# Kernel optimization log

Measured on AMD Instinct MI355X. Metric: run time of the kernel, lower is better.

The kernel has to match this reference:

```python
import jax, jax.numpy as jnp
import numpy as np

W_SIM, W_REC, W_FREQ, W_IMP, W_TYPE = 0.45, 0.2, 0.15, 0.1, 0.1
TYPE_WEIGHT = 0.9
DECAY_HALF_LIFE = 200.0
TEMPERATURE = 0.07
LN_EPS = 1e-5


def _l2norm(v, axis=-1):
    # matches torch F.normalize (eps=1e-12 clamp on the norm)
    n = jnp.linalg.norm(v, axis=axis, keepdims=True)
    return v / jnp.maximum(n, 1e-12)


def setup_inputs() -> dict:
    key = jax.random.key(0)
    ks = jax.random.split(key, 8)
    B, D, S = 16384, 2048, 64
    s = 1.0 / np.sqrt(D)
    x = jax.random.normal(ks[0], (B, D), jnp.float32)
    prototypes = _l2norm(jax.random.normal(ks[1], (S, D), jnp.float32))
    proto_conf = jax.random.uniform(ks[2], (S,), jnp.float32)
    proto_age = jax.random.uniform(ks[3], (S,), jnp.float32)
    proto_evidence = jnp.ones((S,), jnp.float32)
    W_in = jax.random.normal(ks[4], (D, D), jnp.float32) * s
    b_in = jnp.zeros((D,), jnp.float32)
    Wr1 = jax.random.normal(ks[5], (D // 2, D), jnp.float32) * s
    br1 = jnp.zeros((D // 2,), jnp.float32)
    Wr2 = jax.random.normal(ks[6], (4, D // 2), jnp.float32) * (1.0 / np.sqrt(D // 2))
    br2 = jnp.zeros((4,), jnp.float32)
    W_out = jax.random.normal(ks[7], (D, 2 * D), jnp.float32) * (1.0 / np.sqrt(2 * D))
    b_out = jnp.zeros((D,), jnp.float32)
    ln_w = jnp.ones((D,), jnp.float32)
    ln_b = jnp.zeros((D,), jnp.float32)
    return {"x": x, "prototypes": prototypes, "proto_conf": proto_conf,
            "proto_age": proto_age, "proto_evidence": proto_evidence,
            "W_in": W_in, "b_in": b_in, "Wr1": Wr1, "br1": br1,
            "Wr2": Wr2, "br2": br2, "W_out": W_out, "b_out": b_out,
            "ln_w": ln_w, "ln_b": ln_b}


def reference(x, prototypes, proto_conf, proto_age, proto_evidence,
              W_in, b_in, Wr1, br1, Wr2, br2, W_out, b_out, ln_w, ln_b):
    S = prototypes.shape[0]
    protos_per_type = S // 4

    # in_proj + normalize
    h = x @ W_in.T + b_in                                  # [B, D]
    h_norm = _l2norm(h)

    # type router: Linear -> GELU(exact) -> Linear -> softmax
    r = jax.nn.gelu(x @ Wr1.T + br1, approximate=False)    # [B, D/2]
    type_weights = jax.nn.softmax(r @ Wr2.T + br2, axis=-1)  # [B, 4]

    # prototype similarity
    p_norm = _l2norm(prototypes)
    raw_sim = h_norm @ p_norm.T                            # [B, S]

    type_assign = jnp.arange(S) // protos_per_type         # [S] in {0..3}
    type_mask = type_weights[:, type_assign]               # [B, S]
    weighted_sim = raw_sim * type_mask * proto_conf[None, :]

    # multi-factor salience (fused elementwise)
    recency = jnp.exp(-proto_age / DECAY_HALF_LIFE)[None, :]
    freq_norm = (jnp.log(proto_evidence + 1.0) /
                 (jnp.log(proto_evidence.max() + 2.0) + 1e-8))[None, :]
    sal = (W_SIM * weighted_sim + W_REC * recency + W_FREQ * freq_norm
           + W_IMP * proto_conf[None, :] + W_TYPE * TYPE_WEIGHT)
    sal = jnp.clip(sal, 0.0, 1.0)

    # attention over prototype bank
    attn = jax.nn.softmax(sal / TEMPERATURE, axis=-1)       # [B, S]
    retrieved = attn @ prototypes                           # [B, D]

    combined = jnp.concatenate([x, retrieved], axis=-1)     # [B, 2D]
    out = jax.nn.gelu(combined @ W_out.T + b_out, approximate=False)
    # dropout is identity in eval mode

    # residual + LayerNorm (biased variance, eps=1e-5)
    y = out + x
    mu = jnp.mean(y, axis=-1, keepdims=True)
    var = jnp.mean((y - mu) ** 2, axis=-1, keepdims=True)
    return ln_w * (y - mu) / jnp.sqrt(var + LN_EPS) + ln_b
```

## Files before the change

kernel.cpp:

```cpp
#include <hip/hip_runtime.h>
#include <hip/hip_bf16.h>
#include <cstdint>

#define DEV __device__ __forceinline__

typedef __bf16 bf16x8 __attribute__((ext_vector_type(8)));
typedef float f32x4 __attribute__((ext_vector_type(4)));
typedef unsigned short ushort_t;
typedef ushort_t ushort8 __attribute__((ext_vector_type(8)));

DEV ushort_t f2bf(float f) {
  union { float f; uint32_t u; } x; x.f = f;
  uint32_t r = (x.u + 0x7fffu + ((x.u >> 16) & 1u)) >> 16;
  return (ushort_t)r;
}
DEV float bf2f(ushort_t b) {
  union { uint32_t u; float f; } x; x.u = ((uint32_t)b) << 16;
  return x.f;
}
DEV float gelu_exact(float v) {
  return 0.5f * v * (1.0f + erff(v * 0.70710678118654752f));
}
DEV void gload_lds16(const void* g, void* l) {
  __builtin_amdgcn_global_load_lds(
      (const __attribute__((address_space(1))) void*)g,
      (__attribute__((address_space(3))) void*)l, 16, 0, 0);
}


__global__ __launch_bounds__(64) void prep_scal(
    const float* __restrict__ conf, const float* __restrict__ age,
    const float* __restrict__ ev, float* __restrict__ base, float* __restrict__ cs) {
  int l = threadIdx.x;
  float e = ev[l];
  float m = e;
  #pragma unroll
  for (int d = 1; d < 64; d <<= 1) m = fmaxf(m, __shfl_xor(m, d));
  float freq = logf(e + 1.f) / (logf(m + 2.f) + 1e-8f);
  base[l] = 0.2f * expf(-age[l] * (1.f / 200.f)) + 0.15f * freq + 0.1f * conf[l] + 0.09f;
  cs[l] = 0.45f * conf[l];
}

__global__ __launch_bounds__(256) void prep_pnorm(
    const float* __restrict__ protos, const float* __restrict__ b_in,
    float* __restrict__ p_norm, float* __restrict__ dvec) {
  const int s = blockIdx.x, t = threadIdx.x;
  const float* p = protos + (size_t)s * 2048;
  float vals[8];
  float ss = 0.f, sb = 0.f;
  #pragma unroll
  for (int ii = 0; ii < 2; ++ii) {
    float4 v = *(const float4*)(p + t * 8 + ii * 4);
    float4 bi = *(const float4*)(b_in + t * 8 + ii * 4);
    vals[ii * 4 + 0] = v.x; vals[ii * 4 + 1] = v.y; vals[ii * 4 + 2] = v.z; vals[ii * 4 + 3] = v.w;
    ss += v.x * v.x + v.y * v.y + v.z * v.z + v.w * v.w;
    sb += v.x * bi.x + v.y * bi.y + v.z * bi.z + v.w * bi.w;
  }
  #pragma unroll
  for (int d = 1; d < 64; d <<= 1) { ss += __shfl_xor(ss, d); sb += __shfl_xor(sb, d); }
  __shared__ float red[8];
  if ((t & 63) == 0) { red[t >> 6] = ss; red[4 + (t >> 6)] = sb; }
  __syncthreads();
  ss = red[0] + red[1] + red[2] + red[3];
  sb = red[4] + red[5] + red[6] + red[7];
  float inv = 1.f / fmaxf(sqrtf(ss), 1e-12f);
  #pragma unroll
  for (int k = 0; k < 8; ++k) p_norm[(size_t)s * 2048 + t * 8 + k] = vals[k] * inv;
  if (t == 0) dvec[s] = sb * inv;
}


__global__ __launch_bounds__(256) void conv_x(const float* __restrict__ x, ushort_t* __restrict__ xa) {
  size_t e = ((size_t)blockIdx.x * 256 + threadIdx.x) * 8;
  int row = (int)(e >> 11), col = (int)(e & 2047);
  float4 f0 = *(const float4*)(x + e);
  float4 f1 = *(const float4*)(x + e + 4);
  ushort8 o;
  o[0] = f2bf(f0.x); o[1] = f2bf(f0.y); o[2] = f2bf(f0.z); o[3] = f2bf(f0.w);
  o[4] = f2bf(f1.x); o[5] = f2bf(f1.y); o[6] = f2bf(f1.z); o[7] = f2bf(f1.w);
  *(ushort8*)(xa + (size_t)row * 2112 + col) = o;
}

__global__ __launch_bounds__(256) void conv_wbig(const float* __restrict__ W_in,
                                                 const float* __restrict__ Wr1,
                                                 ushort_t* __restrict__ wbig) {
  size_t e = ((size_t)blockIdx.x * 256 + threadIdx.x) * 8;
  int row = (int)(e >> 11), col = (int)(e & 2047);
  if (row >= 3072 && row < 3136) return;
  ushort8 o;
  if (row < 3072) {
    const float* src = (row < 2048) ? (W_in + (size_t)row * 2048 + col)
                                    : (Wr1 + (size_t)(row - 2048) * 2048 + col);
    float4 f0 = *(const float4*)(src);
    float4 f1 = *(const float4*)(src + 4);
    o[0] = f2bf(f0.x); o[1] = f2bf(f0.y); o[2] = f2bf(f0.z); o[3] = f2bf(f0.w);
    o[4] = f2bf(f1.x); o[5] = f2bf(f1.y); o[6] = f2bf(f1.z); o[7] = f2bf(f1.w);
  } else {
    o = ushort8{0, 0, 0, 0, 0, 0, 0, 0};
  }
  *(ushort8*)(wbig + (size_t)row * 2048 + col) = o;
}

__global__ __launch_bounds__(256) void conv_ww(const float* __restrict__ W_out,
                                               ushort_t* __restrict__ wwm) {
  size_t e = ((size_t)blockIdx.x * 256 + threadIdx.x) * 8;
  int n = (int)(e >> 11), c = (int)(e & 2047);
  float4 f0 = *(const float4*)(W_out + (size_t)n * 4096 + c);
  float4 f1 = *(const float4*)(W_out + (size_t)n * 4096 + c + 4);
  ushort8 o;
  o[0] = f2bf(f0.x); o[1] = f2bf(f0.y); o[2] = f2bf(f0.z); o[3] = f2bf(f0.w);
  o[4] = f2bf(f1.x); o[5] = f2bf(f1.y); o[6] = f2bf(f1.z); o[7] = f2bf(f1.w);
  *(ushort8*)(wwm + (size_t)n * 2112 + c) = o;
}

__global__ __launch_bounds__(256) void small_p2(const float* __restrict__ p_norm,
                                                const float* __restrict__ W_in,
                                                ushort_t* __restrict__ wbig) {
  __shared__ float pn[8][128];
  const int t = threadIdx.x;
  const int k = blockIdx.x * 128 + (t & 127);
  const int sh = t >> 7;
  const int s0 = blockIdx.y * 8;
  float acc[4] = {0.f, 0.f, 0.f, 0.f};
  for (int j0 = 0; j0 < 2048; j0 += 128) {
    __syncthreads();
    {
      int sl = t >> 5;
      int j4 = (t & 31) * 4;
      *(float4*)&pn[sl][j4] = *(const float4*)&p_norm[(size_t)(s0 + sl) * 2048 + j0 + j4];
    }
    __syncthreads();
    #pragma unroll 8
    for (int jj = 0; jj < 128; ++jj) {
      float wv = W_in[(size_t)(j0 + jj) * 2048 + k];
      #pragma unroll
      for (int i = 0; i < 4; ++i) acc[i] += pn[sh * 4 + i][jj] * wv;
    }
  }
  #pragma unroll
  for (int i = 0; i < 4; ++i)
    wbig[(size_t)(3072 + s0 + sh * 4 + i) * 2048 + k] = f2bf(acc[i]);
}

__global__ __launch_bounds__(256) void small_R(const float* __restrict__ protos,
                                               const float* __restrict__ W_out,
                                               ushort_t* __restrict__ wwm) {
  __shared__ float pch[64][68];
  __shared__ float wch[16][68];
  const int t = threadIdx.x;
  const int n_loc = t >> 4;
  const int sb = t & 15;
  const int n0 = blockIdx.x * 16;
  float acc[4] = {0.f, 0.f, 0.f, 0.f};
  for (int k0 = 0; k0 < 2048; k0 += 64) {
    __syncthreads();
    #pragma unroll
    for (int ii = 0; ii < 4; ++ii) {
      int lin4 = t * 4 + ii;
      int s = lin4 >> 4;
      int k4 = (lin4 & 15) * 4;
      *(float4*)&pch[s][k4] = *(const float4*)&protos[(size_t)s * 2048 + k0 + k4];
    }
    {
      int n_l = t >> 4;
      int k4 = (t & 15) * 4;
      *(float4*)&wch[n_l][k4] = *(const float4*)&W_out[(size_t)(n0 + n_l) * 4096 + 2048 + k0 + k4];
    }
    __syncthreads();
    #pragma unroll 8
    for (int kk = 0; kk < 64; ++kk) {
      float wv = wch[n_loc][kk];
      #pragma unroll
      for (int i = 0; i < 4; ++i) acc[i] += pch[sb + 16 * i][kk] * wv;
    }
  }
  #pragma unroll
  for (int i = 0; i < 4; ++i)
    wwm[(size_t)(n0 + n_loc) * 2112 + 2048 + sb + 16 * i] = f2bf(acc[i]);
}

template <int MODE>
__global__ __launch_bounds__(256) void gemm_bt(
    const ushort_t* __restrict__ A, int lda,
    const ushort_t* __restrict__ Bw, int ldb, int K,
    const float* __restrict__ bias0, const float* __restrict__ bias1,
    float* __restrict__ out0, ushort_t* __restrict__ out1, float* __restrict__ out2) {
  __shared__ ushort_t As[128 * 32];
  __shared__ ushort_t Bs[128 * 32];
  const int tid = threadIdx.x;
  const int w = tid >> 6, l = tid & 63;
  const int bm = blockIdx.x * 128;
  const int bn = blockIdx.y * 128;
  const int srow = tid >> 2;
  const int scol = (tid & 3) * 8;
  const int wm = (w >> 1) * 64, wn = (w & 1) * 64;
  const int lr = l & 15, lk = (l >> 4) * 8;

  f32x4 acc[4][4];
  #pragma unroll
  for (int i = 0; i < 4; ++i)
    #pragma unroll
    for (int j = 0; j < 4; ++j) acc[i][j] = f32x4{0.f, 0.f, 0.f, 0.f};

  for (int k0 = 0; k0 < K; k0 += 32) {
    __syncthreads();
    #pragma unroll
    for (int r = 0; r < 2; ++r) {
      int row = srow + r * 64;
      gload_lds16(A + (size_t)(bm + row) * lda + k0 + scol,
                  (char*)As + (size_t)(r * 256 + tid) * 16);
    }
    #pragma unroll
    for (int r = 0; r < 2; ++r) {
      int row = srow + r * 64;
      gload_lds16(Bw + (size_t)(bn + row) * ldb + k0 + scol,
                  (char*)Bs + (size_t)(r * 256 + tid) * 16);
    }
    __syncthreads();
    bf16x8 af[4], bf_[4];
    #pragma unroll
    for (int i = 0; i < 4; ++i) af[i] = *(const bf16x8*)&As[(wm + i * 16 + lr) * 32 + lk];
    #pragma unroll
    for (int j = 0; j < 4; ++j) bf_[j] = *(const bf16x8*)&Bs[(wn + j * 16 + lr) * 32 + lk];
    #pragma unroll
    for (int i = 0; i < 4; ++i)
      #pragma unroll
      for (int j = 0; j < 4; ++j)
        acc[i][j] = __builtin_amdgcn_mfma_f32_16x16x32_bf16(af[i], bf_[j], acc[i][j], 0, 0, 0);
  }

  const int lg = l >> 4;
  if constexpr (MODE == 0) {
    #pragma unroll
    for (int i = 0; i < 4; ++i) {
      #pragma unroll
      for (int q = 0; q < 4; ++q) {
        const int grow = bm + wm + i * 16 + lg * 4 + q;
        float ss = 0.f;
        #pragma unroll
        for (int j = 0; j < 4; ++j) {
          const int gcol = bn + wn + j * 16 + lr;
          float v = acc[i][j][q];
          if (gcol < 2048) {
            v += bias0[gcol];
            ss += v * v;
          } else if (gcol < 3072) {
            v += bias1[gcol - 2048];
            out1[(size_t)grow * 1024 + (gcol - 2048)] = f2bf(gelu_exact(v));
          } else if (gcol < 3136) {
            out2[(size_t)grow * 64 + (gcol - 3072)] = v;
          }
        }
        if (bn < 2048) {
          ss += __shfl_xor(ss, 1);
          ss += __shfl_xor(ss, 2);
          ss += __shfl_xor(ss, 4);
          ss += __shfl_xor(ss, 8);
          if (lr == 0) atomicAdd(&out0[grow], ss);
        }
      }
    }
  } else {
    #pragma unroll
    for (int i = 0; i < 4; ++i)
      #pragma unroll
      for (int j = 0; j < 4; ++j)
        #pragma unroll
        for (int q = 0; q < 4; ++q) {
          const int grow = bm + wm + i * 16 + lg * 4 + q;
          const int gcol = bn + wn + j * 16 + lr;
          float v = acc[i][j][q] + bias0[gcol];
          float g = gelu_exact(v);
          out0[(size_t)grow * 2048 + gcol] = g + bias1[(size_t)grow * 2048 + gcol];
        }
  }
}

__global__ __launch_bounds__(256) void attn_k(
    const ushort_t* __restrict__ r_bf, const float* __restrict__ Wr2,
    const float* __restrict__ br2, const float* __restrict__ rn2,
    const float* __restrict__ rproj, const float* __restrict__ dvec,
    const float* __restrict__ base, const float* __restrict__ cs,
    ushort_t* __restrict__ xa) {
  const int b = blockIdx.x * 4 + (threadIdx.x >> 6);
  const int l = threadIdx.x & 63;
  const ushort_t* rrow = r_bf + (size_t)b * 1024;
  float t0 = 0.f, t1 = 0.f, t2 = 0.f, t3 = 0.f;
  #pragma unroll
  for (int m = 0; m < 16; ++m) {
    int k = l + m * 64;
    float rv = bf2f(rrow[k]);
    t0 += rv * Wr2[k];
    t1 += rv * Wr2[1024 + k];
    t2 += rv * Wr2[2048 + k];
    t3 += rv * Wr2[3072 + k];
  }
  #pragma unroll
  for (int d = 1; d < 64; d <<= 1) {
    t0 += __shfl_xor(t0, d); t1 += __shfl_xor(t1, d);
    t2 += __shfl_xor(t2, d); t3 += __shfl_xor(t3, d);
  }
  t0 += br2[0]; t1 += br2[1]; t2 += br2[2]; t3 += br2[3];
  float mx = fmaxf(fmaxf(t0, t1), fmaxf(t2, t3));
  float e0 = expf(t0 - mx), e1 = expf(t1 - mx), e2 = expf(t2 - mx), e3 = expf(t3 - mx);
  float sinv = 1.f / (e0 + e1 + e2 + e3);
  float tw0 = e0 * sinv, tw1 = e1 * sinv, tw2 = e2 * sinv, tw3 = e3 * sinv;
  const int ty = l >> 4;
  float twv = (ty == 0) ? tw0 : ((ty == 1) ? tw1 : ((ty == 2) ? tw2 : tw3));

  float inv = 1.f / fmaxf(sqrtf(rn2[b]), 1e-12f);
  float rp = rproj[(size_t)b * 64 + l] + dvec[l];
  float sal = cs[l] * twv * (rp * inv) + base[l];
  sal = fminf(fmaxf(sal, 0.f), 1.f);
  float logit = sal * (1.f / 0.07f);
  float lm = logit;
  #pragma unroll
  for (int d = 1; d < 64; d <<= 1) lm = fmaxf(lm, __shfl_xor(lm, d));
  float ex = expf(logit - lm);
  float es = ex;
  #pragma unroll
  for (int d = 1; d < 64; d <<= 1) es += __shfl_xor(es, d);
  float attn = ex / es;
  xa[(size_t)b * 2112 + 2048 + l] = f2bf(attn);
}

__global__ __launch_bounds__(256) void ln_k(float* __restrict__ y,
                                            const float* __restrict__ lw,
                                            const float* __restrict__ lb) {
  const int b = blockIdx.x, t = threadIdx.x;
  float* row = y + (size_t)b * 2048;
  float4 v0 = *(const float4*)(row + t * 8);
  float4 v1 = *(const float4*)(row + t * 8 + 4);
  float s = v0.x + v0.y + v0.z + v0.w + v1.x + v1.y + v1.z + v1.w;
  float s2 = v0.x * v0.x + v0.y * v0.y + v0.z * v0.z + v0.w * v0.w +
             v1.x * v1.x + v1.y * v1.y + v1.z * v1.z + v1.w * v1.w;
  #pragma unroll
  for (int d = 1; d < 64; d <<= 1) { s += __shfl_xor(s, d); s2 += __shfl_xor(s2, d); }
  __shared__ float red[8];
  if ((t & 63) == 0) { red[t >> 6] = s; red[4 + (t >> 6)] = s2; }
  __syncthreads();
  float ts = red[0] + red[1] + red[2] + red[3];
  float ts2 = red[4] + red[5] + red[6] + red[7];
  const float mu = ts * (1.f / 2048.f);
  const float inv = 1.f / sqrtf(ts2 * (1.f / 2048.f) - mu * mu + 1e-5f);
  float4 w0 = *(const float4*)(lw + t * 8), w1 = *(const float4*)(lw + t * 8 + 4);
  float4 b0 = *(const float4*)(lb + t * 8), b1 = *(const float4*)(lb + t * 8 + 4);
  float4 o0, o1;
  o0.x = (v0.x - mu) * inv * w0.x + b0.x;
  o0.y = (v0.y - mu) * inv * w0.y + b0.y;
  o0.z = (v0.z - mu) * inv * w0.z + b0.z;
  o0.w = (v0.w - mu) * inv * w0.w + b0.w;
  o1.x = (v1.x - mu) * inv * w1.x + b1.x;
  o1.y = (v1.y - mu) * inv * w1.y + b1.y;
  o1.z = (v1.z - mu) * inv * w1.z + b1.z;
  o1.w = (v1.w - mu) * inv * w1.w + b1.w;
  *(float4*)(row + t * 8) = o0;
  *(float4*)(row + t * 8 + 4) = o1;
}

extern "C" void kernel_launch(void* const* d_in, const int* in_sizes, int n_in,
                              void* d_out, int out_size, void* d_ws, size_t ws_size,
                              hipStream_t stream) {
  const float* x      = (const float*)d_in[0];
  const float* protos = (const float*)d_in[1];
  const float* conf   = (const float*)d_in[2];
  const float* age    = (const float*)d_in[3];
  const float* ev     = (const float*)d_in[4];
  const float* W_in   = (const float*)d_in[5];
  const float* b_in   = (const float*)d_in[6];
  const float* Wr1    = (const float*)d_in[7];
  const float* br1    = (const float*)d_in[8];
  const float* Wr2    = (const float*)d_in[9];
  const float* br2    = (const float*)d_in[10];
  const float* W_out  = (const float*)d_in[11];
  const float* b_out  = (const float*)d_in[12];
  const float* ln_w   = (const float*)d_in[13];
  const float* ln_b   = (const float*)d_in[14];
  float* out = (float*)d_out;

  char* ws = (char*)d_ws;
  size_t off = 0;
  auto take = [&](size_t bytes) {
    char* p = ws + off;
    off = (off + bytes + 255) & ~(size_t)255;
    return p;
  };
  ushort_t* xa    = (ushort_t*)take((size_t)16384 * 2112 * 2);
  ushort_t* wbig  = (ushort_t*)take((size_t)3200 * 2048 * 2);
  ushort_t* wwm   = (ushort_t*)take((size_t)2048 * 2112 * 2);
  ushort_t* rbf   = (ushort_t*)take((size_t)16384 * 1024 * 2);
  float*    rproj = (float*)take((size_t)16384 * 64 * 4);
  float*    rn2   = (float*)take((size_t)16384 * 4);
  float*    pnorm = (float*)take((size_t)64 * 2048 * 4);
  float*    base  = (float*)take(256);
  float*    cs    = (float*)take(256);
  float*    dvec  = (float*)take(256);
  (void)in_sizes; (void)n_in; (void)out_size; (void)ws_size;

  hipMemsetAsync(rn2, 0, 16384 * 4, stream);
  prep_scal<<<1, 64, 0, stream>>>(conf, age, ev, base, cs);
  prep_pnorm<<<64, 256, 0, stream>>>(protos, b_in, pnorm, dvec);
  conv_x<<<16384, 256, 0, stream>>>(x, xa);
  conv_wbig<<<3200, 256, 0, stream>>>(W_in, Wr1, wbig);
  conv_ww<<<2048, 256, 0, stream>>>(W_out, wwm);
  small_p2<<<dim3(16, 8), 256, 0, stream>>>(pnorm, W_in, wbig);
  small_R<<<128, 256, 0, stream>>>(protos, W_out, wwm);
  gemm_bt<0><<<dim3(128, 25), 256, 0, stream>>>(xa, 2112, wbig, 2048, 2048,
                                                b_in, br1, rn2, rbf, rproj);
  attn_k<<<4096, 256, 0, stream>>>(rbf, Wr2, br2, rn2, rproj, dvec, base, cs, xa);
  gemm_bt<1><<<dim3(128, 16), 256, 0, stream>>>(xa, 2112, wwm, 2112, 2112,
                                                b_out, x, out, nullptr, nullptr);
  ln_k<<<16384, 256, 0, stream>>>(out, ln_w, ln_b);
}
```

Measured before the change: 977.5 us.

## Replace 128x128 bf16 GEMM with 256x256 double-buffered, swizzled, staged-MFMA kernel

Replaces the simple 128x128 tile GEMM, which does a single LDS buffer and two barriers per 32-wide K step, with a 512-thread 256x256 tile kernel. The new kernel uses 64-wide K steps, double-buffered LDS filled by global_load_lds, and an XOR swizzle to avoid LDS bank conflicts. Each K tile is split into four MFMA phases interleaved with prefetch of the next A tile and the tile-after-next B tile, with setprio raising MFMA priority. B rows beyond the matrix end are clamped so the 3200-row weight fits 13 column tiles. The change adds a large 128KB LDS footprint and intricate vmcnt accounting, and the padded tile does wasted work.

```diff
diff --git a/kernel.cpp b/kernel.cpp
--- a/kernel.cpp
+++ b/kernel.cpp
@@ -26,6 +26,12 @@
       (const __attribute__((address_space(1))) void*)g,
       (__attribute__((address_space(3))) void*)l, 16, 0, 0);
 }
+DEV void bar() {
+  asm volatile("" ::: "memory");
+  __builtin_amdgcn_s_barrier();
+  asm volatile("" ::: "memory");
+}
+DEV void waitlgkm0() { asm volatile("s_waitcnt lgkmcnt(0)" ::: "memory"); }
 
 
 __global__ __launch_bounds__(64) void prep_scal(
@@ -180,95 +186,192 @@
 }
 
 template <int MODE>
-__global__ __launch_bounds__(256) void gemm_bt(
+__global__ __launch_bounds__(512, 2) void gemm256(
     const ushort_t* __restrict__ A, int lda,
-    const ushort_t* __restrict__ Bw, int ldb, int K,
+    const ushort_t* __restrict__ Bw, int ldb, int K, int Brows,
     const float* __restrict__ bias0, const float* __restrict__ bias1,
     float* __restrict__ out0, ushort_t* __restrict__ out1, float* __restrict__ out2) {
-  __shared__ ushort_t As[128 * 32];
-  __shared__ ushort_t Bs[128 * 32];
-  const int tid = threadIdx.x;
-  const int w = tid >> 6, l = tid & 63;
-  const int bm = blockIdx.x * 128;
-  const int bn = blockIdx.y * 128;
-  const int srow = tid >> 2;
-  const int scol = (tid & 3) * 8;
-  const int wm = (w >> 1) * 64, wn = (w & 1) * 64;
-  const int lr = l & 15, lk = (l >> 4) * 8;
-
-  f32x4 acc[4][4];
-  #pragma unroll
-  for (int i = 0; i < 4; ++i)
+  __shared__ char lds[131072];
+  const int t = threadIdx.x;
+  const int l = t & 63, w = t >> 6;
+  const int wr = w >> 2, wc = w & 3;
+  const int lr = l & 15, lg = l >> 4;
+  const int bm = blockIdx.x * 256;
+  const int bn = blockIdx.y * 256;
+  const int NT = K >> 6;
+
+  const int srow = t >> 3;
+  const int schunk = t & 7;
+  const int gsw = ((schunk ^ (srow & 7)) * 8);
+  const int ldsL = srow * 128 + schunk * 16;
+
+  char* const Ab = lds;
+  char* const Bb = lds + 65536;
+
+  auto stA = [&](int buf, int half, int kt) {
+    const size_t gbase = (size_t)(bm + half * 128 + srow) * lda + (size_t)kt * 64 + gsw;
+    char* const d = Ab + buf * 32768 + half * 16384 + ldsL;
+    gload_lds16(A + gbase, d);
+    gload_lds16(A + gbase + (size_t)64 * lda, d + 8192);
+  };
+  auto stB = [&](int buf, int half, int kt) {
+    int r0 = bn + half * 128 + srow;
+    int r1 = r0 + 64;
+    if (r0 >= Brows) r0 = Brows - 1;
+    if (r1 >= Brows) r1 = Brows - 1;
+    const size_t koff = (size_t)kt * 64 + gsw;
+    char* const d = Bb + buf * 32768 + half * 16384 + ldsL;
+    gload_lds16(Bw + (size_t)r0 * ldb + koff, d);
+    gload_lds16(Bw + (size_t)r1 * ldb + koff, d + 8192);
+  };
+
+  const int q16 = ((lg ^ (lr & 7)) << 4);
+  const int laneA = (wr * 128 + lr) * 128 + q16;
+  const int laneB = (wc * 64 + lr) * 128 + q16;
+
+  f32x4 acc[8][4];
+  #pragma unroll
+  for (int i = 0; i < 8; ++i)
     #pragma unroll
     for (int j = 0; j < 4; ++j) acc[i][j] = f32x4{0.f, 0.f, 0.f, 0.f};
 
-  for (int k0 = 0; k0 < K; k0 += 32) {
-    __syncthreads();
-    #pragma unroll
-    for (int r = 0; r < 2; ++r) {
-      int row = srow + r * 64;
-      gload_lds16(A + (size_t)(bm + row) * lda + k0 + scol,
-                  (char*)As + (size_t)(r * 256 + tid) * 16);
-    }
-    #pragma unroll
-    for (int r = 0; r < 2; ++r) {
-      int row = srow + r * 64;
-      gload_lds16(Bw + (size_t)(bn + row) * ldb + k0 + scol,
-                  (char*)Bs + (size_t)(r * 256 + tid) * 16);
-    }
-    __syncthreads();
-    bf16x8 af[4], bf_[4];
-    #pragma unroll
-    for (int i = 0; i < 4; ++i) af[i] = *(const bf16x8*)&As[(wm + i * 16 + lr) * 32 + lk];
-    #pragma unroll
-    for (int j = 0; j < 4; ++j) bf_[j] = *(const bf16x8*)&Bs[(wn + j * 16 + lr) * 32 + lk];
+  stA(0, 0, 0); stA(0, 1, 0); stB(0, 0, 0); stB(0, 1, 0);
+  stB(1, 0, 1); stB(1, 1, 1);
+  asm volatile("s_waitcnt vmcnt(4)" ::: "memory");
+  bar();
+
+  bf16x8 av[4][2], b0v[2][2], b1v[2][2];
+
+  for (int kt = 0; kt < NT; ++kt) {
+    const int cur = kt & 1, nxt = cur ^ 1;
+    const char* const Ac = Ab + cur * 32768;
+    const char* const Bc = Bb + cur * 32768;
+
+    #pragma unroll
+    for (int i = 0; i < 4; ++i) {
+      av[i][0] = *(const bf16x8*)(Ac + ((laneA + i * 2048) ^ 0));
+      av[i][1] = *(const bf16x8*)(Ac + ((laneA + i * 2048) ^ 64));
+    }
+    #pragma unroll
+    for (int j = 0; j < 2; ++j) {
+      b0v[j][0] = *(const bf16x8*)(Bc + ((laneB + j * 2048) ^ 0));
+      b0v[j][1] = *(const bf16x8*)(Bc + ((laneB + j * 2048) ^ 64));
+    }
+    if (kt + 1 < NT) stA(nxt, 0, kt + 1);
+    bar();
+    waitlgkm0();
+    __builtin_amdgcn_s_setprio(1);
     #pragma unroll
     for (int i = 0; i < 4; ++i)
       #pragma unroll
-      for (int j = 0; j < 4; ++j)
-        acc[i][j] = __builtin_amdgcn_mfma_f32_16x16x32_bf16(af[i], bf_[j], acc[i][j], 0, 0, 0);
-  }
-
-  const int lg = l >> 4;
+      for (int j = 0; j < 2; ++j) {
+        acc[i][j] = __builtin_amdgcn_mfma_f32_16x16x32_bf16(av[i][0], b0v[j][0], acc[i][j], 0, 0, 0);
+        acc[i][j] = __builtin_amdgcn_mfma_f32_16x16x32_bf16(av[i][1], b0v[j][1], acc[i][j], 0, 0, 0);
+      }
+    __builtin_amdgcn_s_setprio(0);
+    bar();
+
+    #pragma unroll
+    for (int j = 0; j < 2; ++j) {
+      b1v[j][0] = *(const bf16x8*)(Bc + ((laneB + (2 + j) * 2048) ^ 0));
+      b1v[j][1] = *(const bf16x8*)(Bc + ((laneB + (2 + j) * 2048) ^ 64));
+    }
+    if (kt + 1 < NT) stA(nxt, 1, kt + 1);
+    bar();
+    waitlgkm0();
+    __builtin_amdgcn_s_setprio(1);
+    #pragma unroll
+    for (int i = 0; i < 4; ++i)
+      #pragma unroll
+      for (int j = 0; j < 2; ++j) {
+        acc[i][2 + j] = __builtin_amdgcn_mfma_f32_16x16x32_bf16(av[i][0], b1v[j][0], acc[i][2 + j], 0, 0, 0);
+        acc[i][2 + j] = __builtin_amdgcn_mfma_f32_16x16x32_bf16(av[i][1], b1v[j][1], acc[i][2 + j], 0, 0, 0);
+      }
+    __builtin_amdgcn_s_setprio(0);
+    bar();
+
+    #pragma unroll
+    for (int i = 0; i < 4; ++i) {
+      av[i][0] = *(const bf16x8*)(Ac + ((laneA + (4 + i) * 2048) ^ 0));
+      av[i][1] = *(const bf16x8*)(Ac + ((laneA + (4 + i) * 2048) ^ 64));
+    }
+    if (kt + 2 < NT) stB(cur, 0, kt + 2);
+    bar();
+    waitlgkm0();
+    __builtin_amdgcn_s_setprio(1);
+    #pragma unroll
+    for (int i = 0; i < 4; ++i)
+      #pragma unroll
+      for (int j = 0; j < 2; ++j) {
+        acc[4 + i][2 + j] = __builtin_amdgcn_mfma_f32_16x16x32_bf16(av[i][0], b1v[j][0], acc[4 + i][2 + j], 0, 0, 0);
+        acc[4 + i][2 + j] = __builtin_amdgcn_mfma_f32_16x16x32_bf16(av[i][1], b1v[j][1], acc[4 + i][2 + j], 0, 0, 0);
+      }
+    __builtin_amdgcn_s_setprio(0);
+    bar();
+
+    if (kt + 2 < NT) stB(cur, 1, kt + 2);
+    bar();
+    __builtin_amdgcn_s_setprio(1);
+    #pragma unroll
+    for (int i = 0; i < 4; ++i)
+      #pragma unroll
+      for (int j = 0; j < 2; ++j) {
+        acc[4 + i][j] = __builtin_amdgcn_mfma_f32_16x16x32_bf16(av[i][0], b0v[j][0], acc[4 + i][j], 0, 0, 0);
+        acc[4 + i][j] = __builtin_amdgcn_mfma_f32_16x16x32_bf16(av[i][1], b0v[j][1], acc[4 + i][j], 0, 0, 0);
+      }
+    __builtin_amdgcn_s_setprio(0);
+    if (kt + 2 < NT) {
+      asm volatile("s_waitcnt vmcnt(4)" ::: "memory");
+    } else if (kt + 1 < NT) {
+      asm volatile("s_waitcnt vmcnt(0)" ::: "memory");
+    }
+    bar();
+  }
+
   if constexpr (MODE == 0) {
     #pragma unroll
-    for (int i = 0; i < 4; ++i) {
+    for (int i = 0; i < 8; ++i) {
       #pragma unroll
       for (int q = 0; q < 4; ++q) {
-        const int grow = bm + wm + i * 16 + lg * 4 + q;
-        float ss = 0.f;
-        #pragma unroll
-        for (int j = 0; j < 4; ++j) {
-          const int gcol = bn + wn + j * 16 + lr;
-          float v = acc[i][j][q];
-          if (gcol < 2048) {
-            v += bias0[gcol];
+        const int grow = bm + wr * 128 + i * 16 + lg * 4 + q;
+        if (bn < 2048) {
+          float ss = 0.f;
+          #pragma unroll
+          for (int j = 0; j < 4; ++j) {
+            const int gcol = bn + wc * 64 + j * 16 + lr;
+            float v = acc[i][j][q] + bias0[gcol];
             ss += v * v;
-          } else if (gcol < 3072) {
-            v += bias1[gcol - 2048];
-            out1[(size_t)grow * 1024 + (gcol - 2048)] = f2bf(gelu_exact(v));
-          } else if (gcol < 3136) {
-            out2[(size_t)grow * 64 + (gcol - 3072)] = v;
           }
-        }
-        if (bn < 2048) {
           ss += __shfl_xor(ss, 1);
           ss += __shfl_xor(ss, 2);
           ss += __shfl_xor(ss, 4);
           ss += __shfl_xor(ss, 8);
           if (lr == 0) atomicAdd(&out0[grow], ss);
+        } else if (bn < 3072) {
+          #pragma unroll
+          for (int j = 0; j < 4; ++j) {
+            const int gcol = bn + wc * 64 + j * 16 + lr;
+            float v = acc[i][j][q] + bias1[gcol - 2048];
+            out1[(size_t)grow * 1024 + (gcol - 2048)] = f2bf(gelu_exact(v));
+          }
+        } else {
+          #pragma unroll
+          for (int j = 0; j < 4; ++j) {
+            const int gcol = bn + wc * 64 + j * 16 + lr;
+            if (gcol < 3136) out2[(size_t)grow * 64 + (gcol - 3072)] = acc[i][j][q];
+          }
         }
       }
     }
   } else {
     #pragma unroll
-    for (int i = 0; i < 4; ++i)
+    for (int i = 0; i < 8; ++i)
       #pragma unroll
       for (int j = 0; j < 4; ++j)
         #pragma unroll
         for (int q = 0; q < 4; ++q) {
-          const int grow = bm + wm + i * 16 + lg * 4 + q;
-          const int gcol = bn + wn + j * 16 + lr;
+          const int grow = bm + wr * 128 + i * 16 + lg * 4 + q;
+          const int gcol = bn + wc * 64 + j * 16 + lr;
           float v = acc[i][j][q] + bias0[gcol];
           float g = gelu_exact(v);
           out0[(size_t)grow * 2048 + gcol] = g + bias1[(size_t)grow * 2048 + gcol];
@@ -405,10 +508,10 @@
   conv_ww<<<2048, 256, 0, stream>>>(W_out, wwm);
   small_p2<<<dim3(16, 8), 256, 0, stream>>>(pnorm, W_in, wbig);
   small_R<<<128, 256, 0, stream>>>(protos, W_out, wwm);
-  gemm_bt<0><<<dim3(128, 25), 256, 0, stream>>>(xa, 2112, wbig, 2048, 2048,
-                                                b_in, br1, rn2, rbf, rproj);
+  gemm256<0><<<dim3(64, 13), 512, 0, stream>>>(xa, 2112, wbig, 2048, 2048, 3200,
+                                               b_in, br1, rn2, rbf, rproj);
   attn_k<<<4096, 256, 0, stream>>>(rbf, Wr2, br2, rn2, rproj, dvec, base, cs, xa);
-  gemm_bt<1><<<dim3(128, 16), 256, 0, stream>>>(xa, 2112, wwm, 2112, 2112,
-                                                b_out, x, out, nullptr, nullptr);
+  gemm256<1><<<dim3(64, 8), 512, 0, stream>>>(xa, 2112, wwm, 2112, 2112, 2048,
+                                              b_out, x, out, nullptr, nullptr);
   ln_k<<<16384, 256, 0, stream>>>(out, ln_w, ln_b);
 }
```

Measured after the change: 996.1 us. About the same (+1.9%).
